# Performance work log

Hardware: AMD Instinct MI355X
Metric: run time of the kernel (lower is better)

The kernel has to match this reference:

```python
import jax, jax.numpy as jnp
import numpy as np

K = 5  # kNN neighbors (includes self, as in PyG knn(x, x, k))


def _lin_bn(x, W, b, s, h):
    # Linear -> ReLU -> BatchNorm (inference, folded to scale s / shift h)
    return jax.nn.relu(x @ W + b) * s + h


def _knn_idx(x, k):
    # x: [B, N, F] -> idx: [B, N, k] indices of k nearest points (incl. self)
    x2 = jnp.sum(x * x, axis=-1)  # [B, N]
    d = x2[:, :, None] + x2[:, None, :] - 2.0 * jnp.einsum('bnf,bmf->bnm', x, x)
    return jax.lax.top_k(-d, k)[1]


def _edge_conv(x, k, edge_mlp):
    # DynamicEdgeConv: knn graph, message mlp([x_i, x_j - x_i]), max-aggregate
    idx = _knn_idx(x, k)                                   # [B, N, k]
    xj = jax.vmap(lambda xb, ib: xb[ib])(x, idx)           # [B, N, k, F]
    xi = jnp.broadcast_to(x[:, :, None, :], xj.shape)
    e = jnp.concatenate([xi, xj - xi], axis=-1)            # [B, N, k, 2F]
    return jnp.max(edge_mlp(e), axis=2)                    # [B, N, F_out]


def _forward(pos, w1a, b1a, s1a, h1a, w1b, b1b, s1b, h1b, w1c, b1c, s1c, h1c,
             w2, b2, s2, h2, wl, bl, sl, hl,
             wm1, bm1, sm1, hm1, wm2, bm2, sm2, hm2, wout, bout):
    mlp1 = lambda e: _lin_bn(_lin_bn(_lin_bn(e, w1a, b1a, s1a, h1a),
                                     w1b, b1b, s1b, h1b), w1c, b1c, s1c, h1c)
    mlp2 = lambda e: _lin_bn(e, w2, b2, s2, h2)
    x1 = _edge_conv(pos, K, mlp1)                          # [B, N, 64]
    x2 = _edge_conv(x1, K, mlp2)                           # [B, N, 128]
    out = _lin_bn(jnp.concatenate([x1, x2], axis=-1), wl, bl, sl, hl)  # [B,N,1024]
    out = jnp.max(out, axis=1)                             # global max pool -> [B,1024]
    out = _lin_bn(out, wm1, bm1, sm1, hm1)                 # Dropout = identity (eval)
    out = _lin_bn(out, wm2, bm2, sm2, hm2)
    return out @ wout + bout                               # [B, n_classes]


def setup_inputs() -> dict:
    key = jax.random.key(0)
    ks = jax.random.split(key, 32)
    B, N = 32, 2048
    rn = lambda k, sh: jax.random.normal(k, sh, dtype=jnp.float32)
    ru = lambda k, sh: jax.random.uniform(k, sh, dtype=jnp.float32)
    d = {'pos': rn(ks[0], (B, N, 3))}
    i = 1
    for nm, cin, cout in [('1a', 6, 64), ('1b', 64, 64), ('1c', 64, 64),
                          ('2', 128, 128), ('l', 192, 1024),
                          ('m1', 1024, 512), ('m2', 512, 256)]:
        d['w' + nm] = rn(ks[i], (cin, cout)) / np.sqrt(cin); i += 1
        d['b' + nm] = rn(ks[i], (cout,)) * 0.1; i += 1
        d['s' + nm] = ru(ks[i], (cout,)) + 0.5; i += 1
        d['h' + nm] = rn(ks[i], (cout,)) * 0.1; i += 1
    d['wout'] = rn(ks[i], (256, 2)) / np.sqrt(256.0); i += 1
    d['bout'] = rn(ks[i], (2,)) * 0.1
    return d


def reference(pos, w1a, b1a, s1a, h1a, w1b, b1b, s1b, h1b, w1c, b1c, s1c, h1c,
              w2, b2, s2, h2, wl, bl, sl, hl,
              wm1, bm1, sm1, hm1, wm2, bm2, sm2, hm2, wout, bout):
    return _forward(pos, w1a, b1a, s1a, h1a, w1b, b1b, s1b, h1b, w1c, b1c, s1c, h1c,
                    w2, b2, s2, h2, wl, bl, sl, hl,
                    wm1, bm1, sm1, hm1, wm2, bm2, sm2, hm2, wout, bout)
```

## Files before the change

kernel.cpp:

```cpp
#include <hip/hip_runtime.h>

#define DEV __device__ __forceinline__
DEV float relu_(float x) { return fmaxf(x, 0.0f); }

typedef __attribute__((ext_vector_type(4))) float f32x4;
typedef __attribute__((ext_vector_type(8))) __bf16 bf16x8;

DEV unsigned short bfbits(__bf16 b) { union { unsigned short s; __bf16 b; } x; x.b = b; return x.s; }
DEV __bf16 bffrom(unsigned short s) { union { unsigned short s; __bf16 b; } x; x.s = s; return x.b; }

DEV void knn_insert(float (&bd)[5], int (&bi)[5], float d, int j) {
  if (d >= bd[4]) return;
  bd[4] = d; bi[4] = j;
#pragma unroll
  for (int p = 4; p > 0; --p) {
    if (bd[p] < bd[p - 1]) {
      float td = bd[p]; bd[p] = bd[p - 1]; bd[p - 1] = td;
      int ti = bi[p]; bi[p] = bi[p - 1]; bi[p - 1] = ti;
    }
  }
}

DEV void knn_insert_bl(float (&bd)[5], int (&bi)[5], float d, int j) {
#pragma unroll
  for (int p = 0; p < 5; ++p) {
    bool lt = d < bd[p];
    float nd = lt ? d : bd[p];
    float cd = lt ? bd[p] : d;
    int ni = lt ? j : bi[p];
    int ci = lt ? bi[p] : j;
    bd[p] = nd; d = cd;
    bi[p] = ni; j = ci;
  }
}

DEV void ins5(float (&b)[5], float x) {
  b[4] = __builtin_amdgcn_fmed3f(b[3], b[4], x);
  b[3] = __builtin_amdgcn_fmed3f(b[2], b[3], x);
  b[2] = __builtin_amdgcn_fmed3f(b[1], b[2], x);
  b[1] = __builtin_amdgcn_fmed3f(b[0], b[1], x);
  b[0] = fminf(b[0], x);
}

DEV void merge_net5(float (&a)[5], float b0, float b1, float b2, float b3, float b4) {
  float c0 = fminf(a[0], b0);
  float c1 = fminf(fminf(b1, a[1]), fmaxf(a[0], b0));
  float c2 = fminf(fminf(b2, a[2]), fminf(fmaxf(a[0], b1), fmaxf(a[1], b0)));
  float c3 = fminf(fminf(b3, a[3]),
                   fminf(fmaxf(a[0], b2), fminf(fmaxf(a[1], b1), fmaxf(a[2], b0))));
  float c4 = fminf(fminf(b4, a[4]),
                   fminf(fminf(fmaxf(a[0], b3), fmaxf(a[1], b2)),
                         fminf(fmaxf(a[2], b1), fmaxf(a[3], b0))));
  a[0] = c0; a[1] = c1; a[2] = c2; a[3] = c3; a[4] = c4;
}

__global__ __launch_bounds__(256) void k_front(
    const float* __restrict__ pos, const float* __restrict__ w1a,
    const float* __restrict__ b1a, const float* __restrict__ w1b,
    const float* __restrict__ w1c, const float* __restrict__ w2,
    const float* __restrict__ wl,
    int* __restrict__ idx1, float* __restrict__ uR, float* __restrict__ vR,
    __bf16* __restrict__ wfh, __bf16* __restrict__ wfl,
    __bf16* __restrict__ wph, __bf16* __restrict__ wpl,
    __bf16* __restrict__ wlb) {
  __shared__ __align__(16) float smem[9472];
  int tid = threadIdx.x;
  int blk = blockIdx.x;
  if (blk < 2048) {
    float* xs = smem;
    float* sqs = smem + 6144;
    float* md = smem + 8192;
    int* mi = (int*)(smem + 8832);
    int b = blk >> 6, qc = blk & 63;
    const float* src = pos + b * 6144;
    for (int u = tid; u < 6144; u += 256) {
      float v = src[u];
      int p = u / 3, c = u - p * 3;
      smem[c * 2048 + p] = v;
    }
    __syncthreads();
    for (int u = tid; u < 2048; u += 256) {
      float x = xs[u], y = xs[2048 + u], z = xs[4096 + u];
      sqs[u] = fmaf(z, z, fmaf(y, y, x * x));
    }
    __syncthreads();
    int q = tid & 31, sub = tid >> 5;
    int qi = qc * 32 + q;
    float qx = xs[qi], qy = xs[2048 + qi], qz = xs[4096 + qi];
    float qsq = sqs[qi];
    float bp[5] = {1e30f, 1e30f, 1e30f, 1e30f, 1e30f};
    int j0 = sub * 256;
    for (int j4 = 0; j4 < 64; ++j4) {
      int jb = j0 + j4 * 4;
      float4 xv = *(const float4*)(xs + jb);
      float4 yv = *(const float4*)(xs + 2048 + jb);
      float4 zv = *(const float4*)(xs + 4096 + jb);
      float4 sv = *(const float4*)(sqs + jb);
      float xa[4] = {xv.x, xv.y, xv.z, xv.w};
      float ya[4] = {yv.x, yv.y, yv.z, yv.w};
      float za[4] = {zv.x, zv.y, zv.z, zv.w};
      float sa[4] = {sv.x, sv.y, sv.z, sv.w};
#pragma unroll
      for (int c = 0; c < 4; ++c) {
        float dot = fmaf(qz, za[c], fmaf(qy, ya[c], qx * xa[c]));
        float d = fmaxf((qsq + sa[c]) - 2.0f * dot, 0.0f);
        unsigned u = (__float_as_uint(d) & 0xFFFFFF00u) | (unsigned)(j4 * 4 + c);
        ins5(bp, __uint_as_float(u));
      }
    }
    float bd[5]; int bi[5];
#pragma unroll
    for (int k = 0; k < 5; ++k) {
      unsigned u = __float_as_uint(bp[k]);
      bd[k] = __uint_as_float(u & 0xFFFFFF00u);
      bi[k] = j0 + (int)(u & 255u);
    }
    for (int half = 4; half >= 1; half >>= 1) {
      __syncthreads();
      if (sub >= half && sub < 2 * half) {
        int slot = (q * 4 + (sub - half)) * 5;
#pragma unroll
        for (int k = 0; k < 5; ++k) { md[slot + k] = bd[k]; mi[slot + k] = bi[k]; }
      }
      __syncthreads();
      if (sub < half) {
        int slot = (q * 4 + sub) * 5;
#pragma unroll
        for (int k = 0; k < 5; ++k) knn_insert_bl(bd, bi, md[slot + k], mi[slot + k]);
      }
    }
    if (sub == 0) {
      int* op = idx1 + (b * 2048 + qi) * 5;
#pragma unroll
      for (int k = 0; k < 5; ++k) op[k] = bi[k];
    }
  } else if (blk < 3072) {
    float* wAs = smem;
    float* bs = smem + 384;
    float* uS = smem + 448;
    float* vS = smem + 4800;
    for (int u = tid; u < 384; u += 256) wAs[u] = w1a[u];
    if (tid < 64) bs[tid] = b1a[tid];
    __syncthreads();
    int lane = tid & 63, fq = tid >> 6;
    int p0 = (blk - 2048) * 64;
    int p = p0 + lane;
    float x0 = pos[p * 3], x1 = pos[p * 3 + 1], x2 = pos[p * 3 + 2];
#pragma unroll
    for (int m = 0; m < 16; ++m) {
      int f = fq * 16 + m;
      float wt0 = wAs[f], wt1 = wAs[64 + f], wt2 = wAs[128 + f];
      float wb0 = wAs[192 + f], wb1 = wAs[256 + f], wb2 = wAs[320 + f];
      float uval = bs[f];
      uval = fmaf(x0, wt0 - wb0, uval);
      uval = fmaf(x1, wt1 - wb1, uval);
      uval = fmaf(x2, wt2 - wb2, uval);
      uS[lane * 68 + f] = uval;
      vS[lane * 68 + f] = fmaf(x2, wb2, fmaf(x1, wb1, x0 * wb0));
    }
    __syncthreads();
#pragma unroll
    for (int it = 0; it < 4; ++it) {
      int g = it * 1024 + tid * 4;
      int pl = g >> 6, f = g & 63;
      float4 uu = *(const float4*)(uS + pl * 68 + f);
      float4 vv = *(const float4*)(vS + pl * 68 + f);
      *(float4*)(uR + (size_t)p0 * 64 + g) = uu;
      *(float4*)(vR + (size_t)p0 * 64 + g) = vv;
    }
  } else {
    int pblk = blk - 3072;
    if (pblk < 4) {
      int t = pblk * 256 + tid;
      int m = t >> 9;
      int rem = t & 511;
      int nb = rem >> 7;
      int rem2 = rem & 127;
      int s = rem2 >> 6, lane = rem2 & 63;
      int k0 = s * 32 + (lane >> 4) * 8;
      int c = nb * 16 + (lane & 15);
      const float* W = m ? w1c : w1b;
      __bf16 oh[8], ol[8];
#pragma unroll
      for (int j = 0; j < 8; ++j) {
        float val = W[(k0 + j) * 64 + c];
        __bf16 h = (__bf16)val;
        oh[j] = h;
        ol[j] = (__bf16)(val - (float)h);
      }
      size_t off = (size_t)m * 4096 + ((size_t)((nb * 2 + s) * 64 + lane)) * 8;
      *(uint4*)(wfh + off) = *(const uint4*)oh;
      *(uint4*)(wfl + off) = *(const uint4*)ol;
    } else if (pblk < 12) {
      int t = (pblk - 4) * 256 + tid;
      int nb = t >> 7;
      int rem = t & 127;
      int ks = rem >> 6, lane = rem & 63;
      int k0 = ks * 32 + (lane >> 4) * 8;
      int col16 = lane & 15;
      __bf16 oh[8], ol[8];
#pragma unroll
      for (int j = 0; j < 8; ++j) {
        int k = k0 + j;
        float val;
        if (nb < 8) {
          int c = nb * 16 + col16;
          val = w2[k * 128 + c] - w2[(64 + k) * 128 + c];
        } else {
          int c = (nb - 8) * 16 + col16;
          val = w2[(64 + k) * 128 + c];
        }
        __bf16 h = (__bf16)val;
        oh[j] = h;
        ol[j] = (__bf16)(val - (float)h);
      }
      *(uint4*)(wph + (size_t)t * 8) = *(const uint4*)oh;
      *(uint4*)(wpl + (size_t)t * 8) = *(const uint4*)ol;
    } else {
      int t = (pblk - 12) * 256 + tid;
      int nt = t / 3072;
      int rem = t - nt * 3072;
      int ks = rem / 512;
      int rem2 = rem - ks * 512;
      int nb = rem2 >> 6, lane = rem2 & 63;
      int k0 = ks * 32 + (lane >> 4) * 8;
      int n = nt * 128 + nb * 16 + (lane & 15);
      __bf16 o[8];
#pragma unroll
      for (int j = 0; j < 8; ++j) o[j] = (__bf16)wl[(k0 + j) * 1024 + n];
      *(uint4*)(wlb + (size_t)t * 8) = *(const uint4*)o;
    }
  }
}

__global__ __launch_bounds__(256) void k_edge1(
    const int* __restrict__ idx1, const float* __restrict__ uR,
    const float* __restrict__ vR,
    const float* __restrict__ s1a, const float* __restrict__ h1a,
    const float* __restrict__ b1b, const float* __restrict__ s1b,
    const float* __restrict__ h1b,
    const float* __restrict__ b1c, const float* __restrict__ s1c,
    const float* __restrict__ h1c,
    const __bf16* __restrict__ wfh, const __bf16* __restrict__ wfl,
    __bf16* __restrict__ xh, __bf16* __restrict__ xl,
    float* __restrict__ sqo, __bf16* __restrict__ xb) {
  __shared__ __align__(16) __bf16 Wh[8192], Wl[8192];
  __shared__ __align__(16) unsigned h2b[4 * 1088];
  int tid = threadIdx.x;
  int w = tid >> 6, lane = tid & 63;
  int quad = lane >> 4, lm = lane & 15;
#pragma unroll
  for (int it = 0; it < 4; ++it) {
    int u4 = it * 256 + tid;
    *(uint4*)(Wh + (size_t)u4 * 8) = *(const uint4*)(wfh + (size_t)u4 * 8);
    *(uint4*)(Wl + (size_t)u4 * 8) = *(const uint4*)(wfl + (size_t)u4 * 8);
  }
  int p0 = blockIdx.x * 64;
  int b = p0 >> 11;
  size_t bb = (size_t)b * 2048;
  int edge = p0 + w * 16 + lm;
  float sA[2][8], hA[2][8];
#pragma unroll
  for (int s = 0; s < 2; ++s)
#pragma unroll
    for (int j = 0; j < 8; ++j) {
      int k = s * 32 + quad * 8 + j;
      sA[s][j] = s1a[k]; hA[s][j] = h1a[k];
    }
  float bB[4], sB[4], hB[4], bC[4], sC[4], hC[4];
#pragma unroll
  for (int nb = 0; nb < 4; ++nb) {
    int c = nb * 16 + lm;
    bB[nb] = b1b[c]; sB[nb] = s1b[c]; hB[nb] = h1b[c];
    bC[nb] = b1c[c]; sC[nb] = s1c[c]; hC[nb] = h1c[c];
  }
  unsigned* h2w = h2b + w * 1088;
  f32x4 mmax[4];
#pragma unroll
  for (int nb = 0; nb < 4; ++nb)
    mmax[nb] = (f32x4){-3.4e38f, -3.4e38f, -3.4e38f, -3.4e38f};
  __syncthreads();
  const float* urow = uR + (size_t)edge * 64;
  for (int kk = 0; kk < 5; ++kk) {
    int jn = idx1[edge * 5 + kk];
    const float* vrow = vR + (bb + jn) * 64;
    bf16x8 Ah[2], Al[2];
#pragma unroll
    for (int s = 0; s < 2; ++s) {
      int off = s * 32 + quad * 8;
      float4 u0 = *(const float4*)(urow + off);
      float4 u1 = *(const float4*)(urow + off + 4);
      float4 v0 = *(const float4*)(vrow + off);
      float4 v1 = *(const float4*)(vrow + off + 4);
      float uv[8] = {u0.x + v0.x, u0.y + v0.y, u0.z + v0.z, u0.w + v0.w,
                     u1.x + v1.x, u1.y + v1.y, u1.z + v1.z, u1.w + v1.w};
      __bf16 th[8], tl[8];
#pragma unroll
      for (int j = 0; j < 8; ++j) {
        float val = relu_(uv[j]) * sA[s][j] + hA[s][j];
        __bf16 hb = (__bf16)val;
        th[j] = hb;
        tl[j] = (__bf16)(val - (float)hb);
      }
      Ah[s] = *(const bf16x8*)th;
      Al[s] = *(const bf16x8*)tl;
    }
#pragma unroll
    for (int nb = 0; nb < 4; ++nb) {
      bf16x8 Bh0 = *(const bf16x8*)(Wh + ((size_t)((nb * 2 + 0) * 64 + lane)) * 8);
      bf16x8 Bh1 = *(const bf16x8*)(Wh + ((size_t)((nb * 2 + 1) * 64 + lane)) * 8);
      bf16x8 Bl0 = *(const bf16x8*)(Wl + ((size_t)((nb * 2 + 0) * 64 + lane)) * 8);
      bf16x8 Bl1 = *(const bf16x8*)(Wl + ((size_t)((nb * 2 + 1) * 64 + lane)) * 8);
      f32x4 a2 = {0.f, 0.f, 0.f, 0.f};
      a2 = __builtin_amdgcn_mfma_f32_16x16x32_bf16(Ah[0], Bh0, a2, 0, 0, 0);
      a2 = __builtin_amdgcn_mfma_f32_16x16x32_bf16(Ah[1], Bh1, a2, 0, 0, 0);
      a2 = __builtin_amdgcn_mfma_f32_16x16x32_bf16(Ah[0], Bl0, a2, 0, 0, 0);
      a2 = __builtin_amdgcn_mfma_f32_16x16x32_bf16(Ah[1], Bl1, a2, 0, 0, 0);
      a2 = __builtin_amdgcn_mfma_f32_16x16x32_bf16(Al[0], Bh0, a2, 0, 0, 0);
      a2 = __builtin_amdgcn_mfma_f32_16x16x32_bf16(Al[1], Bh1, a2, 0, 0, 0);
#pragma unroll
      for (int r = 0; r < 4; ++r) {
        float vv2 = relu_(a2[r] + bB[nb]) * sB[nb] + hB[nb];
        __bf16 hb = (__bf16)vv2;
        __bf16 lb = (__bf16)(vv2 - (float)hb);
        h2w[(quad * 4 + r) * 68 + nb * 16 + lm] =
            (unsigned)bfbits(hb) | ((unsigned)bfbits(lb) << 16);
      }
    }
    bf16x8 A3h[2], A3l[2];
#pragma unroll
    for (int s = 0; s < 2; ++s) {
      const unsigned* rp = h2w + lm * 68 + s * 32 + quad * 8;
      uint4 da = *(const uint4*)rp;
      uint4 db = *(const uint4*)(rp + 4);
      unsigned dw[8] = {da.x, da.y, da.z, da.w, db.x, db.y, db.z, db.w};
      __bf16 th[8], tl[8];
#pragma unroll
      for (int j = 0; j < 8; ++j) {
        th[j] = bffrom((unsigned short)(dw[j] & 0xFFFFu));
        tl[j] = bffrom((unsigned short)(dw[j] >> 16));
      }
      A3h[s] = *(const bf16x8*)th;
      A3l[s] = *(const bf16x8*)tl;
    }
#pragma unroll
    for (int nb = 0; nb < 4; ++nb) {
      bf16x8 Bh0 = *(const bf16x8*)(Wh + 4096 + ((size_t)((nb * 2 + 0) * 64 + lane)) * 8);
      bf16x8 Bh1 = *(const bf16x8*)(Wh + 4096 + ((size_t)((nb * 2 + 1) * 64 + lane)) * 8);
      bf16x8 Bl0 = *(const bf16x8*)(Wl + 4096 + ((size_t)((nb * 2 + 0) * 64 + lane)) * 8);
      bf16x8 Bl1 = *(const bf16x8*)(Wl + 4096 + ((size_t)((nb * 2 + 1) * 64 + lane)) * 8);
      f32x4 a3 = {0.f, 0.f, 0.f, 0.f};
      a3 = __builtin_amdgcn_mfma_f32_16x16x32_bf16(A3h[0], Bh0, a3, 0, 0, 0);
      a3 = __builtin_amdgcn_mfma_f32_16x16x32_bf16(A3h[1], Bh1, a3, 0, 0, 0);
      a3 = __builtin_amdgcn_mfma_f32_16x16x32_bf16(A3h[0], Bl0, a3, 0, 0, 0);
      a3 = __builtin_amdgcn_mfma_f32_16x16x32_bf16(A3h[1], Bl1, a3, 0, 0, 0);
      a3 = __builtin_amdgcn_mfma_f32_16x16x32_bf16(A3l[0], Bh0, a3, 0, 0, 0);
      a3 = __builtin_amdgcn_mfma_f32_16x16x32_bf16(A3l[1], Bh1, a3, 0, 0, 0);
#pragma unroll
      for (int r = 0; r < 4; ++r) mmax[nb][r] = fmaxf(mmax[nb][r], a3[r]);
    }
  }
  float sqp[4] = {0.f, 0.f, 0.f, 0.f};
#pragma unroll
  for (int nb = 0; nb < 4; ++nb) {
    int c = nb * 16 + lm;
#pragma unroll
    for (int r = 0; r < 4; ++r) {
      float vv3 = relu_(mmax[nb][r] + bC[nb]) * sC[nb] + hC[nb];
      sqp[r] = fmaf(vv3, vv3, sqp[r]);
      __bf16 hb = (__bf16)vv3;
      __bf16 lb = (__bf16)(vv3 - (float)hb);
      int n = p0 + w * 16 + quad * 4 + r;
      xh[(size_t)n * 64 + c] = hb;
      xl[(size_t)n * 64 + c] = lb;
      xb[(size_t)n * 192 + c] = hb;
    }
  }
#pragma unroll
  for (int r = 0; r < 4; ++r) {
    float s = sqp[r];
    s += __shfl_xor(s, 1);
    s += __shfl_xor(s, 2);
    s += __shfl_xor(s, 4);
    s += __shfl_xor(s, 8);
    if (lm == 0) sqo[p0 + w * 16 + quad * 4 + r] = s;
  }
}

__global__ __launch_bounds__(256) void k_mid(const __bf16* __restrict__ xh,
                                             const __bf16* __restrict__ xl,
                                             const float* __restrict__ sq,
                                             __bf16* __restrict__ scratch,
                                             const __bf16* __restrict__ wph,
                                             const __bf16* __restrict__ wpl,
                                             __bf16* __restrict__ Pb,
                                             __bf16* __restrict__ Qb) {
  __shared__ __align__(16) float smem[6656];
  int tid = threadIdx.x;
  int w = tid >> 6, lane = tid & 63;
  int quad = lane >> 4, lm = lane & 15;
  if (blockIdx.x < 2048) {
    __bf16* Bh = (__bf16*)smem;
    __bf16* Bl = (__bf16*)(smem + 2304);
    float* sqs = smem + 4608;
    int blk = blockIdx.x;
    int b = blk >> 6;
    int w6 = blk & 63;
    int qc = w6 >> 1, g = w6 & 1;
    int q0 = qc * 64;
    size_t bb = (size_t)b * 2048;
    for (int u = tid; u < 512; u += 256)
      *(float4*)(sqs + u * 4) = *(const float4*)(sq + bb + u * 4);
    const __bf16* qh = xh + (bb + q0 + w * 16 + lm) * 64 + quad * 8;
    const __bf16* ql = xl + (bb + q0 + w * 16 + lm) * 64 + quad * 8;
    bf16x8 Ah0 = *(const bf16x8*)(qh);
    bf16x8 Ah1 = *(const bf16x8*)(qh + 32);
    bf16x8 Al0 = *(const bf16x8*)(ql);
    bf16x8 Al1 = *(const bf16x8*)(ql + 32);
    int nu = tid >> 3, cu = tid & 7;
    const __bf16* ph0 = xh + (bb + (size_t)g * 1024 + nu) * 64 + cu * 8;
    const __bf16* pl0 = xl + (bb + (size_t)g * 1024 + nu) * 64 + cu * 8;
    __bf16* dh0 = Bh + nu * 72 + cu * 8;
    __bf16* dh1 = Bh + (nu + 32) * 72 + cu * 8;
    __bf16* dl0 = Bl + nu * 72 + cu * 8;
    __bf16* dl1 = Bl + (nu + 32) * 72 + cu * 8;
    uint4 rh0 = *(const uint4*)(ph0);
    uint4 rh1 = *(const uint4*)(ph0 + 2048);
    uint4 rl0 = *(const uint4*)(pl0);
    uint4 rl1 = *(const uint4*)(pl0 + 2048);
    __syncthreads();
    float qsq[4];
#pragma unroll
    for (int r = 0; r < 4; ++r) qsq[r] = sqs[q0 + w * 16 + quad * 4 + r];
    float bp[4][5];
#pragma unroll
    for (int r = 0; r < 4; ++r)
#pragma unroll
      for (int k = 0; k < 5; ++k) bp[r][k] = 1e30f;
    for (int it = 0; it < 16; ++it) {
      *(uint4*)dh0 = rh0;
      *(uint4*)dh1 = rh1;
      *(uint4*)dl0 = rl0;
      *(uint4*)dl1 = rl1;
      __syncthreads();
      if (it < 15) {
        const __bf16* p1 = ph0 + (it + 1) * 4096;
        const __bf16* p2 = pl0 + (it + 1) * 4096;
        rh0 = *(const uint4*)(p1);
        rh1 = *(const uint4*)(p1 + 2048);
        rl0 = *(const uint4*)(p2);
        rl1 = *(const uint4*)(p2 + 2048);
      }
      int ct = g * 16 + it;
#pragma unroll
      for (int nt = 0; nt < 4; ++nt) {
        const __bf16* bph = Bh + (nt * 16 + lm) * 72 + quad * 8;
        const __bf16* bpl = Bl + (nt * 16 + lm) * 72 + quad * 8;
        bf16x8 Bh0 = *(const bf16x8*)(bph);
        bf16x8 Bh1 = *(const bf16x8*)(bph + 32);
        bf16x8 Bl0 = *(const bf16x8*)(bpl);
        bf16x8 Bl1 = *(const bf16x8*)(bpl + 32);
        f32x4 acc = {0.f, 0.f, 0.f, 0.f};
        acc = __builtin_amdgcn_mfma_f32_16x16x32_bf16(Ah0, Bh0, acc, 0, 0, 0);
        acc = __builtin_amdgcn_mfma_f32_16x16x32_bf16(Ah1, Bh1, acc, 0, 0, 0);
        acc = __builtin_amdgcn_mfma_f32_16x16x32_bf16(Ah0, Bl0, acc, 0, 0, 0);
        acc = __builtin_amdgcn_mfma_f32_16x16x32_bf16(Ah1, Bl1, acc, 0, 0, 0);
        acc = __builtin_amdgcn_mfma_f32_16x16x32_bf16(Al0, Bh0, acc, 0, 0, 0);
        acc = __builtin_amdgcn_mfma_f32_16x16x32_bf16(Al1, Bh1, acc, 0, 0, 0);
        float csq = sqs[ct * 64 + nt * 16 + lm];
        unsigned key = (unsigned)(it * 4 + nt);
#pragma unroll
        for (int r = 0; r < 4; ++r) {
          float d = fmaxf((qsq[r] + csq) - 2.0f * acc[r], 0.0f);
          unsigned u = (__float_as_uint(d) & 0xFFFFFFC0u) | key;
          ins5(bp[r], __uint_as_float(u));
        }
      }
      __syncthreads();
    }
#pragma unroll
    for (int r = 0; r < 4; ++r)
#pragma unroll
      for (int k = 0; k < 5; ++k) {
        unsigned u = __float_as_uint(bp[r][k]);
        bp[r][k] = __uint_as_float((u & 0xFFFFFF00u) | ((u & 63u) << 2) |
                                   (unsigned)(lm & 3));
      }
#pragma unroll
    for (int m = 1; m <= 2; m <<= 1) {
#pragma unroll
      for (int r = 0; r < 4; ++r) {
        float b0 = __shfl_xor(bp[r][0], m);
        float b1 = __shfl_xor(bp[r][1], m);
        float b2 = __shfl_xor(bp[r][2], m);
        float b3 = __shfl_xor(bp[r][3], m);
        float b4 = __shfl_xor(bp[r][4], m);
        merge_net5(bp[r], b0, b1, b2, b3, b4);
      }
    }
    int lmb = lm & ~3;
    float bd[4][5];
    int bi[4][5];
#pragma unroll
    for (int r = 0; r < 4; ++r)
#pragma unroll
      for (int k = 0; k < 5; ++k) {
        unsigned u = __float_as_uint(bp[r][k]);
        bd[r][k] = __uint_as_float(u & 0xFFFFFF00u);
        unsigned k8 = u & 255u;
        bi[r][k] = (g << 10) | (((int)(k8 >> 2)) << 4) | (lmb | (int)(k8 & 3));
      }
#pragma unroll
    for (int m = 4; m <= 8; m <<= 1) {
#pragma unroll
      for (int r = 0; r < 4; ++r) {
        float od[5]; int oi[5];
#pragma unroll
        for (int k = 0; k < 5; ++k) {
          od[k] = __shfl_xor(bd[r][k], m);
          oi[k] = __shfl_xor(bi[r][k], m);
        }
#pragma unroll
        for (int k = 0; k < 5; ++k) knn_insert(bd[r], bi[r], od[k], oi[k]);
      }
    }
    if (lm == 0) {
#pragma unroll
      for (int r = 0; r < 4; ++r) {
        int qi = q0 + w * 16 + quad * 4 + r;
        uint2* sp = (uint2*)((char*)scratch + (size_t)(bb + qi) * 384 + 128 + g * 40);
#pragma unroll
        for (int k = 0; k < 5; ++k) {
          uint2 v;
          v.x = __float_as_uint(bd[r][k]);
          v.y = (unsigned)bi[r][k];
          sp[k] = v;
        }
      }
    }
  } else {
    __bf16* Wh = (__bf16*)smem;
    __bf16* Wl = (__bf16*)(smem + 2048);
    int n0 = (blockIdx.x - 2048) * 64;
    const __bf16* ah = xh + (size_t)(n0 + w * 16 + lm) * 64 + quad * 8;
    const __bf16* al = xl + (size_t)(n0 + w * 16 + lm) * 64 + quad * 8;
    bf16x8 Ah0 = *(const bf16x8*)(ah);
    bf16x8 Ah1 = *(const bf16x8*)(ah + 32);
    bf16x8 Al0 = *(const bf16x8*)(al);
    bf16x8 Al1 = *(const bf16x8*)(al + 32);
    for (int chunk = 0; chunk < 4; ++chunk) {
      __syncthreads();
#pragma unroll
      for (int it = 0; it < 2; ++it) {
        int unit = it * 256 + tid;
        *(uint4*)(Wh + (size_t)unit * 8) =
            *(const uint4*)(wph + (size_t)chunk * 4096 + (size_t)unit * 8);
        *(uint4*)(Wl + (size_t)unit * 8) =
            *(const uint4*)(wpl + (size_t)chunk * 4096 + (size_t)unit * 8);
      }
      __syncthreads();
#pragma unroll
      for (int nb4 = 0; nb4 < 4; ++nb4) {
        int nb = chunk * 4 + nb4;
        bf16x8 Bh0 = *(const bf16x8*)(Wh + ((size_t)(nb4 * 2 + 0) * 64 + lane) * 8);
        bf16x8 Bh1 = *(const bf16x8*)(Wh + ((size_t)(nb4 * 2 + 1) * 64 + lane) * 8);
        bf16x8 Bl0 = *(const bf16x8*)(Wl + ((size_t)(nb4 * 2 + 0) * 64 + lane) * 8);
        bf16x8 Bl1 = *(const bf16x8*)(Wl + ((size_t)(nb4 * 2 + 1) * 64 + lane) * 8);
        f32x4 acc = {0.f, 0.f, 0.f, 0.f};
        acc = __builtin_amdgcn_mfma_f32_16x16x32_bf16(Ah0, Bh0, acc, 0, 0, 0);
        acc = __builtin_amdgcn_mfma_f32_16x16x32_bf16(Ah1, Bh1, acc, 0, 0, 0);
        acc = __builtin_amdgcn_mfma_f32_16x16x32_bf16(Ah0, Bl0, acc, 0, 0, 0);
        acc = __builtin_amdgcn_mfma_f32_16x16x32_bf16(Ah1, Bl1, acc, 0, 0, 0);
        acc = __builtin_amdgcn_mfma_f32_16x16x32_bf16(Al0, Bh0, acc, 0, 0, 0);
        acc = __builtin_amdgcn_mfma_f32_16x16x32_bf16(Al1, Bh1, acc, 0, 0, 0);
        bool isP = (nb < 8);
        __bf16* base = isP ? Pb : Qb;
        int col = (isP ? nb : nb - 8) * 16 + lm;
#pragma unroll
        for (int r = 0; r < 4; ++r) {
          int n = n0 + w * 16 + quad * 4 + r;
          base[(size_t)n * 128 + col] = (__bf16)acc[r];
        }
      }
    }
  }
}

__global__ __launch_bounds__(256) void k_kmerge(const __bf16* __restrict__ scratch,
                                                int* __restrict__ idx2) {
  int n = blockIdx.x * 256 + threadIdx.x;
  const uint2* sp = (const uint2*)((const char*)scratch + (size_t)n * 384 + 128);
  float bd[5]; int bi[5];
#pragma unroll
  for (int k = 0; k < 5; ++k) {
    uint2 v = sp[k];
    bd[k] = __uint_as_float(v.x);
    bi[k] = (int)v.y;
  }
#pragma unroll
  for (int k = 0; k < 5; ++k) {
    uint2 v = sp[5 + k];
    knn_insert(bd, bi, __uint_as_float(v.x), (int)v.y);
  }
  int* op = idx2 + (size_t)n * 5;
#pragma unroll
  for (int k = 0; k < 5; ++k) op[k] = bi[k];
}

__global__ __launch_bounds__(256) void k_gmax(const __bf16* __restrict__ Pb,
                                              const __bf16* __restrict__ Qb,
                                              const int* __restrict__ idx2,
                                              const float* __restrict__ b2,
                                              const float* __restrict__ s2,
                                              const float* __restrict__ h2v,
                                              __bf16* __restrict__ xb) {
  int tid = threadIdx.x;
  int c4 = tid & 31, p = tid >> 5;
  int n = blockIdx.x * 8 + p;
  int b = n >> 11;
  const int* ip = idx2 + n * 5;
  int c0 = c4 * 4;
  float m[4] = {-3.4e38f, -3.4e38f, -3.4e38f, -3.4e38f};
#pragma unroll
  for (int k = 0; k < 5; ++k) {
    int j = ip[k];
    uint2 q = *(const uint2*)(Qb + ((size_t)(b * 2048 + j)) * 128 + c0);
    m[0] = fmaxf(m[0], (float)bffrom((unsigned short)(q.x & 0xFFFFu)));
    m[1] = fmaxf(m[1], (float)bffrom((unsigned short)(q.x >> 16)));
    m[2] = fmaxf(m[2], (float)bffrom((unsigned short)(q.y & 0xFFFFu)));
    m[3] = fmaxf(m[3], (float)bffrom((unsigned short)(q.y >> 16)));
  }
  uint2 pv = *(const uint2*)(Pb + (size_t)n * 128 + c0);
  float pvf[4] = {(float)bffrom((unsigned short)(pv.x & 0xFFFFu)),
                  (float)bffrom((unsigned short)(pv.x >> 16)),
                  (float)bffrom((unsigned short)(pv.y & 0xFFFFu)),
                  (float)bffrom((unsigned short)(pv.y >> 16))};
  __bf16 o[4];
#pragma unroll
  for (int i = 0; i < 4; ++i) {
    float v = pvf[i] + m[i] + b2[c0 + i];
    o[i] = (__bf16)(relu_(v) * s2[c0 + i] + h2v[c0 + i]);
  }
  uint2 ov;
  ov.x = (unsigned)bfbits(o[0]) | ((unsigned)bfbits(o[1]) << 16);
  ov.y = (unsigned)bfbits(o[2]) | ((unsigned)bfbits(o[3]) << 16);
  *(uint2*)(xb + (size_t)n * 192 + 64 + c0) = ov;
}

__global__ __launch_bounds__(256) void k_linl_mfma(const __bf16* __restrict__ xb,
                                                   const __bf16* __restrict__ wlb,
                                                   float* __restrict__ pool_part) {
  __shared__ __align__(16) __bf16 Aall[12288];
  __shared__ __align__(16) __bf16 Bl[8192];
  int tid = threadIdx.x;
  int w = tid >> 6, lane = tid & 63;
  int mg = blockIdx.x;
  int n0 = mg << 6;
  int quad = lane >> 4, lm = lane & 15;
#pragma unroll
  for (int it = 0; it < 6; ++it) {
    int unit = it * 256 + tid;
    int mb = unit / 384;
    int rem = unit - mb * 384;
    int ks = rem >> 6, ln = rem & 63;
    int lmm = ln & 15, qd = ln >> 4;
    const uint4* ga = (const uint4*)(xb + (size_t)(n0 + mb * 16 + lmm) * 192 + ks * 32 + qd * 8);
    *(uint4*)(Aall + ((size_t)(mb * 6 + ks) * 64 + ln) * 8) = *ga;
  }
  for (int ng = 0; ng < 4; ++ng) {
    f32x4 acc[4][4];
#pragma unroll
    for (int i = 0; i < 4; ++i)
#pragma unroll
      for (int j = 0; j < 4; ++j) acc[i][j] = (f32x4){0.f, 0.f, 0.f, 0.f};
    for (int ks = 0; ks < 6; ++ks) {
      __syncthreads();
#pragma unroll
      for (int nt2 = 0; nt2 < 2; ++nt2) {
#pragma unroll
        for (int u = 0; u < 2; ++u) {
          int unit = u * 256 + tid;
          const uint4* gb = (const uint4*)(wlb + ((size_t)((ng * 2 + nt2) * 6 + ks)) * 4096 + (size_t)unit * 8);
          *(uint4*)(Bl + (size_t)nt2 * 4096 + (size_t)unit * 8) = *gb;
        }
      }
      __syncthreads();
      bf16x8 af[4], bfr[4];
#pragma unroll
      for (int i = 0; i < 4; ++i)
        af[i] = *(const bf16x8*)(Aall + ((size_t)(i * 6 + ks) * 64 + lane) * 8);
      int nt2 = w >> 1, nbb = (w & 1) * 4;
#pragma unroll
      for (int j = 0; j < 4; ++j)
        bfr[j] = *(const bf16x8*)(Bl + (size_t)nt2 * 4096 + ((size_t)((nbb + j) * 64 + lane)) * 8);
#pragma unroll
      for (int i = 0; i < 4; ++i)
#pragma unroll
        for (int j = 0; j < 4; ++j)
          acc[i][j] = __builtin_amdgcn_mfma_f32_16x16x32_bf16(af[i], bfr[j], acc[i][j], 0, 0, 0);
    }
#pragma unroll
    for (int j = 0; j < 4; ++j) {
      float m = -3.4e38f;
#pragma unroll
      for (int i = 0; i < 4; ++i)
#pragma unroll
        for (int r = 0; r < 4; ++r) m = fmaxf(m, acc[i][j][r]);
      m = fmaxf(m, __shfl_xor(m, 16));
      m = fmaxf(m, __shfl_xor(m, 32));
      if (quad == 0) {
        int ch = ng * 256 + (w >> 1) * 128 + (w & 1) * 64 + j * 16 + lm;
        pool_part[(size_t)mg * 1024 + ch] = m;
      }
    }
  }
}

__global__ __launch_bounds__(256) void k_pool(const float* __restrict__ pool_part,
                                              const float* __restrict__ bl,
                                              const float* __restrict__ sl,
                                              const float* __restrict__ hl,
                                              float* __restrict__ p,
                                              float* __restrict__ out) {
  int b = blockIdx.x >> 2, cb = blockIdx.x & 3;
  int c = cb * 256 + threadIdx.x;
  const float* src = pool_part + (size_t)(b * 32) * 1024 + c;
  float m0 = -3.4e38f, m1 = -3.4e38f, m2 = -3.4e38f, m3 = -3.4e38f;
#pragma unroll
  for (int t = 0; t < 32; t += 4) {
    m0 = fmaxf(m0, src[(size_t)t * 1024]);
    m1 = fmaxf(m1, src[(size_t)(t + 1) * 1024]);
    m2 = fmaxf(m2, src[(size_t)(t + 2) * 1024]);
    m3 = fmaxf(m3, src[(size_t)(t + 3) * 1024]);
  }
  float m = fmaxf(fmaxf(m0, m1), fmaxf(m2, m3));
  p[b * 1024 + c] = relu_(m + bl[c]) * sl[c] + hl[c];
  if (blockIdx.x == 0 && threadIdx.x < 64) out[threadIdx.x] = 0.0f;
}

__global__ __launch_bounds__(256) void k_m1(const float* __restrict__ p,
                                            const float* __restrict__ wm1,
                                            const float* __restrict__ bm1,
                                            const float* __restrict__ sm1,
                                            const float* __restrict__ hm1,
                                            float* __restrict__ h1) {
  __shared__ float p_s[1024];
  __shared__ float red[4][64];
  int b = blockIdx.x >> 3, cb = blockIdx.x & 7;
  int tid = threadIdx.x;
  for (int u = tid; u < 1024; u += 256) p_s[u] = p[b * 1024 + u];
  __syncthreads();
  int c64 = tid & 63, q = tid >> 6;
  int C = cb * 64 + c64;
  int f0 = q * 256;
  const float* W = wm1 + (size_t)f0 * 512 + C;
  float a[8] = {0.f, 0.f, 0.f, 0.f, 0.f, 0.f, 0.f, 0.f};
  for (int f = 0; f < 256; f += 8) {
#pragma unroll
    for (int u = 0; u < 8; ++u)
      a[u] = fmaf(p_s[f0 + f + u], W[(size_t)(f + u) * 512], a[u]);
  }
  red[q][c64] = ((a[0] + a[1]) + (a[2] + a[3])) + ((a[4] + a[5]) + (a[6] + a[7]));
  __syncthreads();
  if (tid < 64) {
    float t = (red[0][tid] + red[1][tid]) + (red[2][tid] + red[3][tid]);
    int C2 = cb * 64 + tid;
    h1[b * 512 + C2] = relu_(t + bm1[C2]) * sm1[C2] + hm1[C2];
  }
}

__global__ __launch_bounds__(256) void k_m2o(const float* __restrict__ h1,
                                             const float* __restrict__ wm2,
                                             const float* __restrict__ bm2,
                                             const float* __restrict__ sm2,
                                             const float* __restrict__ hm2,
                                             const float* __restrict__ wout,
                                             const float* __restrict__ bout,
                                             float* __restrict__ out) {
  __shared__ float h1_s[512];
  __shared__ float red[4][64];
  int b = blockIdx.x >> 2, cb = blockIdx.x & 3;
  int tid = threadIdx.x;
  for (int u = tid; u < 512; u += 256) h1_s[u] = h1[b * 512 + u];
  __syncthreads();
  int c64 = tid & 63, q = tid >> 6;
  int C = cb * 64 + c64;
  int f0 = q * 128;
  const float* W = wm2 + (size_t)f0 * 256 + C;
  float a[4] = {0.f, 0.f, 0.f, 0.f};
  for (int f = 0; f < 128; f += 4) {
#pragma unroll
    for (int u = 0; u < 4; ++u)
      a[u] = fmaf(h1_s[f0 + f + u], W[(size_t)(f + u) * 256], a[u]);
  }
  red[q][c64] = (a[0] + a[1]) + (a[2] + a[3]);
  __syncthreads();
  if (tid < 64) {
    float t = (red[0][tid] + red[1][tid]) + (red[2][tid] + red[3][tid]);
    int C2 = cb * 64 + tid;
    float h2v = relu_(t + bm2[C2]) * sm2[C2] + hm2[C2];
    float2 wv = *(const float2*)(wout + C2 * 2);
    float v0 = h2v * wv.x, v1 = h2v * wv.y;
#pragma unroll
    for (int m = 1; m < 64; m <<= 1) {
      v0 += __shfl_xor(v0, m);
      v1 += __shfl_xor(v1, m);
    }
    if (tid == 0) {
      if (cb == 0) { v0 += bout[0]; v1 += bout[1]; }
      atomicAdd(&out[b * 2], v0);
      atomicAdd(&out[b * 2 + 1], v1);
    }
  }
}

extern "C" void kernel_launch(void* const* d_in, const int* in_sizes, int n_in,
                              void* d_out, int out_size, void* d_ws, size_t ws_size,
                              hipStream_t stream) {
  const float* pos = (const float*)d_in[0];
  const float* w1a = (const float*)d_in[1];
  const float* b1a = (const float*)d_in[2];
  const float* s1a = (const float*)d_in[3];
  const float* h1a = (const float*)d_in[4];
  const float* w1b = (const float*)d_in[5];
  const float* b1b = (const float*)d_in[6];
  const float* s1b = (const float*)d_in[7];
  const float* h1b = (const float*)d_in[8];
  const float* w1c = (const float*)d_in[9];
  const float* b1c = (const float*)d_in[10];
  const float* s1c = (const float*)d_in[11];
  const float* h1c = (const float*)d_in[12];
  const float* w2 = (const float*)d_in[13];
  const float* b2 = (const float*)d_in[14];
  const float* s2 = (const float*)d_in[15];
  const float* h2 = (const float*)d_in[16];
  const float* wl = (const float*)d_in[17];
  const float* bl = (const float*)d_in[18];
  const float* sl = (const float*)d_in[19];
  const float* hl = (const float*)d_in[20];
  const float* wm1 = (const float*)d_in[21];
  const float* bm1 = (const float*)d_in[22];
  const float* sm1 = (const float*)d_in[23];
  const float* hm1 = (const float*)d_in[24];
  const float* wm2 = (const float*)d_in[25];
  const float* bm2 = (const float*)d_in[26];
  const float* sm2 = (const float*)d_in[27];
  const float* hm2 = (const float*)d_in[28];
  const float* wout = (const float*)d_in[29];
  const float* bout = (const float*)d_in[30];
  float* out = (float*)d_out;

  float* base = (float*)d_ws;
  __bf16* xh = (__bf16*)base;
  __bf16* xl = (__bf16*)(base + 2097152);
  float* PbF = base + 4194304;
  float* QbF = PbF + 4194304;
  float* xbF = QbF + 4194304;
  int* idx = (int*)(xbF + 6291456);
  float* sq = (float*)(idx + 327680);
  __bf16* wph = (__bf16*)(sq + 65536);
  __bf16* wpl = (__bf16*)(sq + 65536 + 8192);
  __bf16* wfh = (__bf16*)(sq + 65536 + 16384);
  __bf16* wfl = (__bf16*)(sq + 65536 + 20480);
  __bf16* wlb = (__bf16*)(sq + 65536 + 24576);
  __bf16* Pb = (__bf16*)PbF;
  __bf16* Qb = (__bf16*)QbF;
  __bf16* xb = (__bf16*)xbF;
  float* uR = PbF;
  float* vR = QbF;
  float* pool_part = base + 131072;
  float* p_pool = base + 1179648;
  float* h1g = base + 1212416;

  k_front<<<3180, 256, 0, stream>>>(pos, w1a, b1a, w1b, w1c, w2, wl, idx, uR, vR,
                                    wfh, wfl, wph, wpl, wlb);
  k_edge1<<<1024, 256, 0, stream>>>(idx, uR, vR, s1a, h1a, b1b, s1b, h1b, b1c,
                                    s1c, h1c, wfh, wfl, xh, xl, sq, xb);
  k_mid<<<3072, 256, 0, stream>>>(xh, xl, sq, xb, wph, wpl, Pb, Qb);
  k_kmerge<<<256, 256, 0, stream>>>(xb, idx);
  k_gmax<<<8192, 256, 0, stream>>>(Pb, Qb, idx, b2, s2, h2, xb);
  k_linl_mfma<<<1024, 256, 0, stream>>>(xb, wlb, pool_part);
  k_pool<<<128, 256, 0, stream>>>(pool_part, bl, sl, hl, p_pool, out);
  k_m1<<<256, 256, 0, stream>>>(p_pool, wm1, bm1, sm1, hm1, h1g);
  k_m2o<<<128, 256, 0, stream>>>(h1g, wm2, bm2, sm2, hm2, wout, bout, out);
}
```

Measured before the change: 356.9 us.

## Process 128 queries per kNN block to reuse staged candidate tiles

The kNN part of k_mid now gives each warp two 16-query tiles, 128 queries per block instead of 64, so each candidate tile staged in shared memory feeds twice as many MFMA computations. This halves the number of kNN blocks and the global and LDS traffic spent loading candidate tiles. In exchange it raises register pressure (8x5 top-k lists plus a second set of A fragments), which may lower occupancy, and it leaves fewer blocks to spread across the GPU.

```diff
diff --git a/kernel.cpp b/kernel.cpp
--- a/kernel.cpp
+++ b/kernel.cpp
@@ -399,24 +399,28 @@
   int tid = threadIdx.x;
   int w = tid >> 6, lane = tid & 63;
   int quad = lane >> 4, lm = lane & 15;
-  if (blockIdx.x < 2048) {
+  if (blockIdx.x < 1024) {
     __bf16* Bh = (__bf16*)smem;
     __bf16* Bl = (__bf16*)(smem + 2304);
     float* sqs = smem + 4608;
     int blk = blockIdx.x;
-    int b = blk >> 6;
-    int w6 = blk & 63;
-    int qc = w6 >> 1, g = w6 & 1;
-    int q0 = qc * 64;
+    int b = blk >> 5;
+    int w5 = blk & 31;
+    int qc = w5 >> 1, g = w5 & 1;
+    int q0 = qc * 128;
     size_t bb = (size_t)b * 2048;
     for (int u = tid; u < 512; u += 256)
       *(float4*)(sqs + u * 4) = *(const float4*)(sq + bb + u * 4);
-    const __bf16* qh = xh + (bb + q0 + w * 16 + lm) * 64 + quad * 8;
-    const __bf16* ql = xl + (bb + q0 + w * 16 + lm) * 64 + quad * 8;
-    bf16x8 Ah0 = *(const bf16x8*)(qh);
-    bf16x8 Ah1 = *(const bf16x8*)(qh + 32);
-    bf16x8 Al0 = *(const bf16x8*)(ql);
-    bf16x8 Al1 = *(const bf16x8*)(ql + 32);
+    const __bf16* qh0 = xh + (bb + q0 + w * 32 + lm) * 64 + quad * 8;
+    const __bf16* ql0 = xl + (bb + q0 + w * 32 + lm) * 64 + quad * 8;
+    bf16x8 Ah0a = *(const bf16x8*)(qh0);
+    bf16x8 Ah1a = *(const bf16x8*)(qh0 + 32);
+    bf16x8 Al0a = *(const bf16x8*)(ql0);
+    bf16x8 Al1a = *(const bf16x8*)(ql0 + 32);
+    bf16x8 Ah0b = *(const bf16x8*)(qh0 + 1024);
+    bf16x8 Ah1b = *(const bf16x8*)(qh0 + 1056);
+    bf16x8 Al0b = *(const bf16x8*)(ql0 + 1024);
+    bf16x8 Al1b = *(const bf16x8*)(ql0 + 1056);
     int nu = tid >> 3, cu = tid & 7;
     const __bf16* ph0 = xh + (bb + (size_t)g * 1024 + nu) * 64 + cu * 8;
     const __bf16* pl0 = xl + (bb + (size_t)g * 1024 + nu) * 64 + cu * 8;
@@ -429,12 +433,15 @@
     uint4 rl0 = *(const uint4*)(pl0);
     uint4 rl1 = *(const uint4*)(pl0 + 2048);
     __syncthreads();
-    float qsq[4];
-#pragma unroll
-    for (int r = 0; r < 4; ++r) qsq[r] = sqs[q0 + w * 16 + quad * 4 + r];
-    float bp[4][5];
-#pragma unroll
-    for (int r = 0; r < 4; ++r)
+    float qsq[8];
+#pragma unroll
+    for (int r = 0; r < 4; ++r) {
+      qsq[r] = sqs[q0 + w * 32 + quad * 4 + r];
+      qsq[4 + r] = sqs[q0 + w * 32 + 16 + quad * 4 + r];
+    }
+    float bp[8][5];
+#pragma unroll
+    for (int r = 0; r < 8; ++r)
 #pragma unroll
       for (int k = 0; k < 5; ++k) bp[r][k] = 1e30f;
     for (int it = 0; it < 16; ++it) {
@@ -460,26 +467,36 @@
         bf16x8 Bh1 = *(const bf16x8*)(bph + 32);
         bf16x8 Bl0 = *(const bf16x8*)(bpl);
         bf16x8 Bl1 = *(const bf16x8*)(bpl + 32);
-        f32x4 acc = {0.f, 0.f, 0.f, 0.f};
-        acc = __builtin_amdgcn_mfma_f32_16x16x32_bf16(Ah0, Bh0, acc, 0, 0, 0);
-        acc = __builtin_amdgcn_mfma_f32_16x16x32_bf16(Ah1, Bh1, acc, 0, 0, 0);
-        acc = __builtin_amdgcn_mfma_f32_16x16x32_bf16(Ah0, Bl0, acc, 0, 0, 0);
-        acc = __builtin_amdgcn_mfma_f32_16x16x32_bf16(Ah1, Bl1, acc, 0, 0, 0);
-        acc = __builtin_amdgcn_mfma_f32_16x16x32_bf16(Al0, Bh0, acc, 0, 0, 0);
-        acc = __builtin_amdgcn_mfma_f32_16x16x32_bf16(Al1, Bh1, acc, 0, 0, 0);
+        f32x4 acc0 = {0.f, 0.f, 0.f, 0.f};
+        acc0 = __builtin_amdgcn_mfma_f32_16x16x32_bf16(Ah0a, Bh0, acc0, 0, 0, 0);
+        acc0 = __builtin_amdgcn_mfma_f32_16x16x32_bf16(Ah1a, Bh1, acc0, 0, 0, 0);
+        acc0 = __builtin_amdgcn_mfma_f32_16x16x32_bf16(Ah0a, Bl0, acc0, 0, 0, 0);
+        acc0 = __builtin_amdgcn_mfma_f32_16x16x32_bf16(Ah1a, Bl1, acc0, 0, 0, 0);
+        acc0 = __builtin_amdgcn_mfma_f32_16x16x32_bf16(Al0a, Bh0, acc0, 0, 0, 0);
+        acc0 = __builtin_amdgcn_mfma_f32_16x16x32_bf16(Al1a, Bh1, acc0, 0, 0, 0);
+        f32x4 acc1 = {0.f, 0.f, 0.f, 0.f};
+        acc1 = __builtin_amdgcn_mfma_f32_16x16x32_bf16(Ah0b, Bh0, acc1, 0, 0, 0);
+        acc1 = __builtin_amdgcn_mfma_f32_16x16x32_bf16(Ah1b, Bh1, acc1, 0, 0, 0);
+        acc1 = __builtin_amdgcn_mfma_f32_16x16x32_bf16(Ah0b, Bl0, acc1, 0, 0, 0);
+        acc1 = __builtin_amdgcn_mfma_f32_16x16x32_bf16(Ah1b, Bl1, acc1, 0, 0, 0);
+        acc1 = __builtin_amdgcn_mfma_f32_16x16x32_bf16(Al0b, Bh0, acc1, 0, 0, 0);
+        acc1 = __builtin_amdgcn_mfma_f32_16x16x32_bf16(Al1b, Bh1, acc1, 0, 0, 0);
         float csq = sqs[ct * 64 + nt * 16 + lm];
         unsigned key = (unsigned)(it * 4 + nt);
 #pragma unroll
         for (int r = 0; r < 4; ++r) {
-          float d = fmaxf((qsq[r] + csq) - 2.0f * acc[r], 0.0f);
-          unsigned u = (__float_as_uint(d) & 0xFFFFFFC0u) | key;
-          ins5(bp[r], __uint_as_float(u));
+          float d0 = fmaxf((qsq[r] + csq) - 2.0f * acc0[r], 0.0f);
+          unsigned u0 = (__float_as_uint(d0) & 0xFFFFFFC0u) | key;
+          ins5(bp[r], __uint_as_float(u0));
+          float d1 = fmaxf((qsq[4 + r] + csq) - 2.0f * acc1[r], 0.0f);
+          unsigned u1 = (__float_as_uint(d1) & 0xFFFFFFC0u) | key;
+          ins5(bp[4 + r], __uint_as_float(u1));
         }
       }
       __syncthreads();
     }
 #pragma unroll
-    for (int r = 0; r < 4; ++r)
+    for (int r = 0; r < 8; ++r)
 #pragma unroll
       for (int k = 0; k < 5; ++k) {
         unsigned u = __float_as_uint(bp[r][k]);
@@ -489,7 +506,7 @@
 #pragma unroll
     for (int m = 1; m <= 2; m <<= 1) {
 #pragma unroll
-      for (int r = 0; r < 4; ++r) {
+      for (int r = 0; r < 8; ++r) {
         float b0 = __shfl_xor(bp[r][0], m);
         float b1 = __shfl_xor(bp[r][1], m);
         float b2 = __shfl_xor(bp[r][2], m);
@@ -499,49 +516,52 @@
       }
     }
     int lmb = lm & ~3;
-    float bd[4][5];
-    int bi[4][5];
-#pragma unroll
-    for (int r = 0; r < 4; ++r)
-#pragma unroll
-      for (int k = 0; k < 5; ++k) {
-        unsigned u = __float_as_uint(bp[r][k]);
-        bd[r][k] = __uint_as_float(u & 0xFFFFFF00u);
-        unsigned k8 = u & 255u;
-        bi[r][k] = (g << 10) | (((int)(k8 >> 2)) << 4) | (lmb | (int)(k8 & 3));
-      }
-#pragma unroll
-    for (int m = 4; m <= 8; m <<= 1) {
-#pragma unroll
-      for (int r = 0; r < 4; ++r) {
-        float od[5]; int oi[5];
+#pragma unroll
+    for (int s = 0; s < 2; ++s) {
+      float bd[4][5];
+      int bi[4][5];
+#pragma unroll
+      for (int r = 0; r < 4; ++r)
 #pragma unroll
         for (int k = 0; k < 5; ++k) {
-          od[k] = __shfl_xor(bd[r][k], m);
-          oi[k] = __shfl_xor(bi[r][k], m);
+          unsigned u = __float_as_uint(bp[s * 4 + r][k]);
+          bd[r][k] = __uint_as_float(u & 0xFFFFFF00u);
+          unsigned k8 = u & 255u;
+          bi[r][k] = (g << 10) | (((int)(k8 >> 2)) << 4) | (lmb | (int)(k8 & 3));
         }
 #pragma unroll
-        for (int k = 0; k < 5; ++k) knn_insert(bd[r], bi[r], od[k], oi[k]);
-      }
-    }
-    if (lm == 0) {
-#pragma unroll
-      for (int r = 0; r < 4; ++r) {
-        int qi = q0 + w * 16 + quad * 4 + r;
-        uint2* sp = (uint2*)((char*)scratch + (size_t)(bb + qi) * 384 + 128 + g * 40);
-#pragma unroll
-        for (int k = 0; k < 5; ++k) {
-          uint2 v;
-          v.x = __float_as_uint(bd[r][k]);
-          v.y = (unsigned)bi[r][k];
-          sp[k] = v;
+      for (int m = 4; m <= 8; m <<= 1) {
+#pragma unroll
+        for (int r = 0; r < 4; ++r) {
+          float od[5]; int oi[5];
+#pragma unroll
+          for (int k = 0; k < 5; ++k) {
+            od[k] = __shfl_xor(bd[r][k], m);
+            oi[k] = __shfl_xor(bi[r][k], m);
+          }
+#pragma unroll
+          for (int k = 0; k < 5; ++k) knn_insert(bd[r], bi[r], od[k], oi[k]);
+        }
+      }
+      if (lm == 0) {
+#pragma unroll
+        for (int r = 0; r < 4; ++r) {
+          int qi = q0 + w * 32 + s * 16 + quad * 4 + r;
+          uint2* sp = (uint2*)((char*)scratch + (size_t)(bb + qi) * 384 + 128 + g * 40);
+#pragma unroll
+          for (int k = 0; k < 5; ++k) {
+            uint2 v;
+            v.x = __float_as_uint(bd[r][k]);
+            v.y = (unsigned)bi[r][k];
+            sp[k] = v;
+          }
         }
       }
     }
   } else {
     __bf16* Wh = (__bf16*)smem;
     __bf16* Wl = (__bf16*)(smem + 2048);
-    int n0 = (blockIdx.x - 2048) * 64;
+    int n0 = (blockIdx.x - 1024) * 64;
     const __bf16* ah = xh + (size_t)(n0 + w * 16 + lm) * 64 + quad * 8;
     const __bf16* al = xl + (size_t)(n0 + w * 16 + lm) * 64 + quad * 8;
     bf16x8 Ah0 = *(const bf16x8*)(ah);
@@ -876,7 +896,7 @@
                                     wfh, wfl, wph, wpl, wlb);
   k_edge1<<<1024, 256, 0, stream>>>(idx, uR, vR, s1a, h1a, b1b, s1b, h1b, b1c,
                                     s1c, h1c, wfh, wfl, xh, xl, sq, xb);
-  k_mid<<<3072, 256, 0, stream>>>(xh, xl, sq, xb, wph, wpl, Pb, Qb);
+  k_mid<<<2048, 256, 0, stream>>>(xh, xl, sq, xb, wph, wpl, Pb, Qb);
   k_kmerge<<<256, 256, 0, stream>>>(xb, idx);
   k_gmax<<<8192, 256, 0, stream>>>(Pb, Qb, idx, b2, s2, h2, xb);
   k_linl_mfma<<<1024, 256, 0, stream>>>(xb, wlb, pool_part);
```

Result: slower. 366.4 us (+2.7%).
